# Kernel tuning notes

Hardware: AMD Instinct MI355X
Metric: run time of the kernel (lower is better)

The kernel has to match this reference:

```python
import jax, jax.numpy as jnp
import numpy as np

THRESHOLD = 0.1  # init arg; module uses threshold**2


def setup_inputs() -> dict:
    key = jax.random.key(0)
    batched_kps = jax.random.normal(key, (131072, 17, 3), dtype=jnp.float32)
    return {"batched_kps": batched_kps}


def reference(batched_kps):
    thr2 = jnp.float32(THRESHOLD ** 2)
    n_joints = batched_kps.shape[1]
    # pairwise squared distances: [B, J, J]
    diff = batched_kps[:, :, None, :] - batched_kps[:, None, :, :]
    d2 = jnp.sum(diff * diff, axis=-1)
    hinge = jnp.maximum(0.0, thr2 - d2)
    # exclude i == j pairs (original loops skip other_joint == joint_i)
    off_diag = ~jnp.eye(n_joints, dtype=bool)
    hinge = jnp.where(off_diag[None, :, :], hinge, 0.0)
    per_batch = jnp.sum(hinge, axis=(1, 2))  # sum over all ordered pairs
    return jnp.mean(per_batch)
```

## Files before the change

kernel.cpp:

```cpp
#include <hip/hip_runtime.h>


#define NJ      17
#define KPF     51
#define BPB     256
#define THREADS 256

__global__ __launch_bounds__(THREADS)
void sep_loss_kernel(const float* __restrict__ kps,
                     float* __restrict__ out,
                     int B, float thr2, float invB) {
    __shared__ float lds[BPB * KPF];
    __shared__ float wsum[THREADS / 64];

    const int tid = threadIdx.x;
    const long long b0 = (long long)blockIdx.x * BPB;

    const float4* __restrict__ src4 =
        reinterpret_cast<const float4*>(kps + b0 * KPF);
    float4* dst4 = reinterpret_cast<float4*>(lds);
    const int n4 = BPB * KPF / 4;
    for (int i = tid; i < n4; i += THREADS) dst4[i] = src4[i];
    __syncthreads();

    float kp[KPF];
    const float* my = lds + tid * KPF;
    #pragma unroll
    for (int k = 0; k < KPF; ++k) kp[k] = my[k];

    float acc = 0.0f;
    #pragma unroll
    for (int i = 0; i < NJ; ++i) {
        #pragma unroll
        for (int j = i + 1; j < NJ; ++j) {
            float dx = kp[i * 3 + 0] - kp[j * 3 + 0];
            float dy = kp[i * 3 + 1] - kp[j * 3 + 1];
            float dz = kp[i * 3 + 2] - kp[j * 3 + 2];
            float d2 = fmaf(dx, dx, fmaf(dy, dy, dz * dz));
            acc += fmaxf(thr2 - d2, 0.0f);
        }
    }
    acc *= 2.0f;

    #pragma unroll
    for (int off = 32; off > 0; off >>= 1)
        acc += __shfl_down(acc, off, 64);
    if ((tid & 63) == 0) wsum[tid >> 6] = acc;
    __syncthreads();

    if (tid == 0) {
        float s = 0.0f;
        #pragma unroll
        for (int w = 0; w < THREADS / 64; ++w) s += wsum[w];
        atomicAdd(out, s * invB);
    }
}

extern "C" void kernel_launch(void* const* d_in, const int* in_sizes, int n_in,
                              void* d_out, int out_size, void* d_ws, size_t ws_size,
                              hipStream_t stream) {
    const float* kps = (const float*)d_in[0];
    float* out = (float*)d_out;

    const int B = in_sizes[0] / KPF;
    const float thr2 = 0.1f * 0.1f;
    const float invB = 1.0f / (float)B;

    hipMemsetAsync(d_out, 0, out_size * sizeof(float), stream);

    const int grid = B / BPB;
    sep_loss_kernel<<<grid, THREADS, 0, stream>>>(kps, out, B, thr2, invB);
}
```

Baseline: 76.35 us.

## Expand squared distance into dot products and shrink blocks to one wavefront

Rewrites the pairwise squared distance as |a|^2+|b|^2-2a·b, precomputing per-joint norms folded with half the threshold, so each pair costs three FMAs plus an add and a max instead of subtractions and squares. Blocks shrink to a single 64-thread wavefront, which removes the shared-memory cross-warp reduction and one barrier but multiplies the number of atomics on the output by four. The norm expansion can lose precision through cancellation when points are close, which is exactly the regime the hinge is sensitive to.

```diff
diff --git a/kernel.cpp b/kernel.cpp
--- a/kernel.cpp
+++ b/kernel.cpp
@@ -3,15 +3,14 @@
 
 #define NJ      17
 #define KPF     51
-#define BPB     256
-#define THREADS 256
+#define BPB     64
+#define THREADS 64
 
 __global__ __launch_bounds__(THREADS)
 void sep_loss_kernel(const float* __restrict__ kps,
                      float* __restrict__ out,
-                     int B, float thr2, float invB) {
+                     float scale , float thr2) {
     __shared__ float lds[BPB * KPF];
-    __shared__ float wsum[THREADS / 64];
 
     const int tid = threadIdx.x;
     const long long b0 = (long long)blockIdx.x * BPB;
@@ -20,6 +19,7 @@
         reinterpret_cast<const float4*>(kps + b0 * KPF);
     float4* dst4 = reinterpret_cast<float4*>(lds);
     const int n4 = BPB * KPF / 4;
+    #pragma unroll
     for (int i = tid; i < n4; i += THREADS) dst4[i] = src4[i];
     __syncthreads();
 
@@ -28,32 +28,31 @@
     #pragma unroll
     for (int k = 0; k < KPF; ++k) kp[k] = my[k];
 
+    float m[NJ];
+    #pragma unroll
+    for (int i = 0; i < NJ; ++i) {
+        float x = kp[i * 3], y = kp[i * 3 + 1], z = kp[i * 3 + 2];
+        m[i] = 0.5f * thr2 - fmaf(x, x, fmaf(y, y, z * z));
+    }
+
     float acc = 0.0f;
     #pragma unroll
     for (int i = 0; i < NJ; ++i) {
         #pragma unroll
         for (int j = i + 1; j < NJ; ++j) {
-            float dx = kp[i * 3 + 0] - kp[j * 3 + 0];
-            float dy = kp[i * 3 + 1] - kp[j * 3 + 1];
-            float dz = kp[i * 3 + 2] - kp[j * 3 + 2];
-            float d2 = fmaf(dx, dx, fmaf(dy, dy, dz * dz));
-            acc += fmaxf(thr2 - d2, 0.0f);
+            float dot = fmaf(kp[i * 3],     kp[j * 3],
+                       fmaf(kp[i * 3 + 1], kp[j * 3 + 1],
+                            kp[i * 3 + 2] * kp[j * 3 + 2]));
+            float v = fmaf(2.0f, dot, m[i] + m[j]);
+            acc += fmaxf(v, 0.0f);
         }
     }
-    acc *= 2.0f;
 
     #pragma unroll
     for (int off = 32; off > 0; off >>= 1)
         acc += __shfl_down(acc, off, 64);
-    if ((tid & 63) == 0) wsum[tid >> 6] = acc;
-    __syncthreads();
-
-    if (tid == 0) {
-        float s = 0.0f;
-        #pragma unroll
-        for (int w = 0; w < THREADS / 64; ++w) s += wsum[w];
-        atomicAdd(out, s * invB);
-    }
+    if (tid == 0)
+        atomicAdd(out, acc * scale);
 }
 
 extern "C" void kernel_launch(void* const* d_in, const int* in_sizes, int n_in,
@@ -64,10 +63,10 @@
 
     const int B = in_sizes[0] / KPF;
     const float thr2 = 0.1f * 0.1f;
-    const float invB = 1.0f / (float)B;
+    const float scale = 2.0f / (float)B;
 
     hipMemsetAsync(d_out, 0, out_size * sizeof(float), stream);
 
     const int grid = B / BPB;
-    sep_loss_kernel<<<grid, THREADS, 0, stream>>>(kps, out, B, thr2, invB);
+    sep_loss_kernel<<<grid, THREADS, 0, stream>>>(kps, out, scale, thr2);
 }
```

After: 97.43 us. 1.28x slower.
